# Optimization experiments

Measured on AMD Instinct MI355X. Metric: run time of the kernel, lower is better.

The kernel has to match this reference:

```python
import jax, jax.numpy as jnp
import numpy as np

HEADS = 8
DH = 160
LN_EPS = 1e-5


def _ln(x):
    m = jnp.mean(x, axis=-1, keepdims=True)
    v = jnp.var(x, axis=-1, keepdims=True)
    return (x - m) * jax.lax.rsqrt(v + LN_EPS)


def _adaln(x, table, w, b, t):
    # table[t]: [dim]; emb -> [2*dim]; chunk along dim 0 (scalar timestep)
    emb = jax.nn.silu(table[t]) @ w + b
    scale, shift = jnp.split(emb, 2)
    return _ln(x) * (1.0 + scale) + shift


def _attn(x, ctx, wq, wk, wv, wo, bo):
    B, S, _ = x.shape
    Sk = ctx.shape[1]
    q = (x @ wq).reshape(B, S, HEADS, DH).transpose(0, 2, 1, 3)    # [B,H,S,dh]
    k = (ctx @ wk).reshape(B, Sk, HEADS, DH).transpose(0, 2, 1, 3)
    v = (ctx @ wv).reshape(B, Sk, HEADS, DH).transpose(0, 2, 1, 3)
    scores = jnp.einsum('bhid,bhjd->bhij', q, k) * (DH ** -0.5)
    probs = jax.nn.softmax(scores, axis=-1)
    o = jnp.einsum('bhij,bhjd->bhid', probs, v)
    o = o.transpose(0, 2, 1, 3).reshape(B, S, HEADS * DH)
    return o @ wo + bo


def _ff(x, w1, b1, w2, b2):
    h, gate = jnp.split(x @ w1 + b1, 2, axis=-1)
    return (h * jax.nn.gelu(gate, approximate=False)) @ w2 + b2


def setup_inputs() -> dict:
    key = jax.random.key(0)
    ks = jax.random.split(key, 24)
    B, S, SC, DIM, CROSS, INNER = 2, 2048, 77, 1280, 768, 5120

    def w(k, shape, s=0.02):
        return jax.random.normal(k, shape, jnp.float32) * s

    return {
        'hidden_states': jax.random.normal(ks[0], (B, S, DIM), jnp.float32),
        'context': jax.random.normal(ks[1], (B, SC, CROSS), jnp.float32),
        'ada1_emb': w(ks[2], (1000, DIM)),
        'ada1_w': w(ks[3], (DIM, 2 * DIM)),
        'ada1_b': jnp.zeros((2 * DIM,), jnp.float32),
        'ada2_emb': w(ks[4], (1000, DIM)),
        'ada2_w': w(ks[5], (DIM, 2 * DIM)),
        'ada2_b': jnp.zeros((2 * DIM,), jnp.float32),
        'a1_wq': w(ks[6], (DIM, DIM)), 'a1_wk': w(ks[7], (DIM, DIM)),
        'a1_wv': w(ks[8], (DIM, DIM)), 'a1_wo': w(ks[9], (DIM, DIM)),
        'a1_bo': jnp.zeros((DIM,), jnp.float32),
        'a2_wq': w(ks[10], (DIM, DIM)), 'a2_wk': w(ks[11], (CROSS, DIM)),
        'a2_wv': w(ks[12], (CROSS, DIM)), 'a2_wo': w(ks[13], (DIM, DIM)),
        'a2_bo': jnp.zeros((DIM,), jnp.float32),
        'norm3_g': jnp.ones((DIM,), jnp.float32),
        'norm3_b': jnp.zeros((DIM,), jnp.float32),
        'ff_w1': w(ks[14], (DIM, 2 * INNER)),
        'ff_b1': jnp.zeros((2 * INNER,), jnp.float32),
        'ff_w2': w(ks[15], (INNER, DIM)),
        'ff_b2': jnp.zeros((DIM,), jnp.float32),
        'timestep': 500,
    }


def reference(hidden_states, context, ada1_emb, ada1_w, ada1_b, ada2_emb, ada2_w, ada2_b,
              a1_wq, a1_wk, a1_wv, a1_wo, a1_bo, a2_wq, a2_wk, a2_wv, a2_wo, a2_bo,
              norm3_g, norm3_b, ff_w1, ff_b1, ff_w2, ff_b2, timestep):
    x = hidden_states
    # self-attention with AdaLayerNorm
    h = _adaln(x, ada1_emb, ada1_w, ada1_b, timestep)
    x = x + _attn(h, h, a1_wq, a1_wk, a1_wv, a1_wo, a1_bo)
    # cross-attention with AdaLayerNorm
    h = _adaln(x, ada2_emb, ada2_w, ada2_b, timestep)
    x = x + _attn(h, context, a2_wq, a2_wk, a2_wv, a2_wo, a2_bo)
    # feed-forward with affine LayerNorm
    h = _ln(x) * norm3_g + norm3_b
    x = x + _ff(h, ff_w1, ff_b1, ff_w2, ff_b2)
    return x
```

## Files before the change

kernel.cpp:

```cpp
#include <hip/hip_runtime.h>

typedef __attribute__((ext_vector_type(8))) unsigned short ushort8;
typedef __attribute__((ext_vector_type(4))) float f32x4;
typedef __attribute__((ext_vector_type(8))) __bf16 bf16x8;
typedef unsigned short u16;

__device__ inline unsigned short f2bf(float f) {
  unsigned u = __float_as_uint(f);
  unsigned r = (u + 0x7fffu + ((u >> 16) & 1u)) >> 16;
  return (unsigned short)r;
}
__device__ inline float bf2f(unsigned short h) {
  return __uint_as_float(((unsigned)h) << 16);
}

__device__ __forceinline__ void gload_lds16(const void* g, void* l) {
  __builtin_amdgcn_global_load_lds(
      (const __attribute__((address_space(1))) void*)g,
      (__attribute__((address_space(3))) void*)l, 16, 0, 0);
}

__device__ __forceinline__ void decomp_bid(int nbx, int nby, int& z, int& bx, int& by) {
  int bid = blockIdx.x;
  const int nwg = gridDim.x;
  const int q8 = nwg >> 3, r8 = nwg & 7;
  const int xcd = bid & 7, i = bid >> 3;
  bid = (xcd < r8 ? xcd * (q8 + 1) : r8 * (q8 + 1) + (xcd - r8) * q8) + i;
  const int nbb = nbx * nby;
  z = bid / nbb;
  int rem = bid - z * nbb;
  if ((nby & 7) == 0) {
    const int chunk = nbx << 3;
    const int c = rem / chunk, w = rem - c * chunk;
    bx = w >> 3;
    by = (c << 3) + (w & 7);
  } else {
    by = rem / nbx;
    bx = rem - by * nbx;
  }
}

__global__ __launch_bounds__(512, 2) void flash_self(
    const u16* __restrict__ qkv, const u16* __restrict__ vtg, u16* __restrict__ o)
{
  __shared__ __align__(128) u16 Qs[128 * 168];
  __shared__ __align__(128) u16 Ks[2][64 * 168];
  __shared__ __align__(128) u16 Vs[2][160 * 64];
  __shared__ __align__(128) u16 Ps[128 * 64];

  const int tid = threadIdx.x;
  const int lane = tid & 63, wave = tid >> 6;
  const int r15 = lane & 15, kq = lane >> 4;
  const int z = blockIdx.x >> 4, qt = blockIdx.x & 15;
  const int b = z >> 3, hh = z & 7;
  const u16* Qg = qkv + ((long)(b * 2048 + qt * 128)) * 3840 + hh * 160;
  const u16* Kg = qkv + ((long)(b * 2048)) * 3840 + 1280 + hh * 160;
  const u16* Vg = vtg + (long)z * 160 * 2048;

  for (int c = tid; c < 2560; c += 512) {
    const int r = c / 20, e = (c % 20) * 8;
    *(ushort8*)&Qs[r * 168 + e] = *(const ushort8*)(Qg + (long)r * 3840 + e);
  }
  const int c0 = tid, c1 = tid + 512, c2 = tid + 1024;
  const bool has2 = (c2 < 1280);
  const int kR0 = c0 / 20, kE0 = (c0 % 20) * 8;
  const int kR1 = c1 / 20, kE1 = (c1 % 20) * 8;
  const int kR2 = has2 ? c2 / 20 : 0, kE2 = has2 ? (c2 % 20) * 8 : 0;
  const int vR0 = c0 >> 3, vG0 = c0 & 7;
  const int vR1 = c1 >> 3, vG1 = c1 & 7;
  const int vR2 = has2 ? (c2 >> 3) : 0, vG2 = has2 ? (c2 & 7) : 0;

  {
    ushort8 k0 = *(const ushort8*)(Kg + (long)kR0 * 3840 + kE0);
    ushort8 k1 = *(const ushort8*)(Kg + (long)kR1 * 3840 + kE1);
    ushort8 v0 = *(const ushort8*)(Vg + (long)vR0 * 2048 + vG0 * 8);
    ushort8 v1 = *(const ushort8*)(Vg + (long)vR1 * 2048 + vG1 * 8);
    *(ushort8*)&Ks[0][kR0 * 168 + kE0] = k0;
    *(ushort8*)&Ks[0][kR1 * 168 + kE1] = k1;
    *(ushort8*)&Vs[0][vR0 * 64 + ((vG0 ^ (vR0 & 7)) * 8)] = v0;
    *(ushort8*)&Vs[0][vR1 * 64 + ((vG1 ^ (vR1 & 7)) * 8)] = v1;
    if (has2) {
      ushort8 k2 = *(const ushort8*)(Kg + (long)kR2 * 3840 + kE2);
      ushort8 v2 = *(const ushort8*)(Vg + (long)vR2 * 2048 + vG2 * 8);
      *(ushort8*)&Ks[0][kR2 * 168 + kE2] = k2;
      *(ushort8*)&Vs[0][vR2 * 64 + ((vG2 ^ (vR2 & 7)) * 8)] = v2;
    }
  }
  __syncthreads();

  bf16x8 qf[5];
#pragma unroll
  for (int kf = 0; kf < 5; ++kf)
    qf[kf] = *(const bf16x8*)&Qs[(wave * 16 + r15) * 168 + kf * 32 + kq * 8];

  float m[4], l[4] = {0.f, 0.f, 0.f, 0.f};
#pragma unroll
  for (int t = 0; t < 4; ++t) m[t] = -1e30f;
  f32x4 accO[10] = {};
  const float SC = 0.07905694150420949f;

  ushort8 kr0, kr1, kr2, vr0, vr1, vr2;

  for (int step = 0; step < 32; ++step) {
    const int cur = step & 1;
    const bool nl = step < 31;
    if (nl) {
      const long kv1 = (long)(step + 1) * 64;
      kr0 = *(const ushort8*)(Kg + (kv1 + kR0) * 3840 + kE0);
      kr1 = *(const ushort8*)(Kg + (kv1 + kR1) * 3840 + kE1);
      vr0 = *(const ushort8*)(Vg + (long)vR0 * 2048 + kv1 + vG0 * 8);
      vr1 = *(const ushort8*)(Vg + (long)vR1 * 2048 + kv1 + vG1 * 8);
      if (has2) {
        kr2 = *(const ushort8*)(Kg + (kv1 + kR2) * 3840 + kE2);
        vr2 = *(const ushort8*)(Vg + (long)vR2 * 2048 + kv1 + vG2 * 8);
      }
    }
    f32x4 sa[4] = {};
#pragma unroll
    for (int nf = 0; nf < 4; ++nf)
#pragma unroll
      for (int kf = 0; kf < 5; ++kf) {
        const bf16x8 kfrag =
            *(const bf16x8*)&Ks[cur][(nf * 16 + r15) * 168 + kf * 32 + kq * 8];
        sa[nf] = __builtin_amdgcn_mfma_f32_16x16x32_bf16(qf[kf], kfrag, sa[nf], 0, 0, 0);
      }
    float corr[4];
#pragma unroll
    for (int t = 0; t < 4; ++t) {
      float tm = fmaxf(fmaxf(sa[0][t], sa[1][t]), fmaxf(sa[2][t], sa[3][t])) * SC;
      tm = fmaxf(tm, __shfl_xor(tm, 1, 64));
      tm = fmaxf(tm, __shfl_xor(tm, 2, 64));
      tm = fmaxf(tm, __shfl_xor(tm, 4, 64));
      tm = fmaxf(tm, __shfl_xor(tm, 8, 64));
      const float mn = fmaxf(m[t], tm);
      corr[t] = __expf(m[t] - mn);
      m[t] = mn;
    }
    const int qr0 = wave * 16 + kq * 4;
#pragma unroll
    for (int t = 0; t < 4; ++t) {
      float rs = 0.f;
      const int qr = qr0 + t;
#pragma unroll
      for (int nf = 0; nf < 4; ++nf) {
        const float p = __expf(sa[nf][t] * SC - m[t]);
        rs += p;
        const int col = r15 + nf * 16;
        Ps[qr * 64 + (((col >> 3) ^ (qr & 7)) * 8) + (col & 7)] = f2bf(p);
      }
      rs += __shfl_xor(rs, 1, 64);
      rs += __shfl_xor(rs, 2, 64);
      rs += __shfl_xor(rs, 4, 64);
      rs += __shfl_xor(rs, 8, 64);
      l[t] = l[t] * corr[t] + rs;
    }
#pragma unroll
    for (int j = 0; j < 10; ++j)
#pragma unroll
      for (int t = 0; t < 4; ++t) accO[j][t] *= corr[t];
    if (nl) {
      const int nxt = cur ^ 1;
      *(ushort8*)&Ks[nxt][kR0 * 168 + kE0] = kr0;
      *(ushort8*)&Ks[nxt][kR1 * 168 + kE1] = kr1;
      *(ushort8*)&Vs[nxt][vR0 * 64 + ((vG0 ^ (vR0 & 7)) * 8)] = vr0;
      *(ushort8*)&Vs[nxt][vR1 * 64 + ((vG1 ^ (vR1 & 7)) * 8)] = vr1;
      if (has2) {
        *(ushort8*)&Ks[nxt][kR2 * 168 + kE2] = kr2;
        *(ushort8*)&Vs[nxt][vR2 * 64 + ((vG2 ^ (vR2 & 7)) * 8)] = vr2;
      }
    }
    __syncthreads();
    const int arow = wave * 16 + r15;
    bf16x8 pf[2];
#pragma unroll
    for (int k2 = 0; k2 < 2; ++k2)
      pf[k2] = *(const bf16x8*)&Ps[arow * 64 + (((k2 * 4 + kq) ^ (arow & 7)) * 8)];
#pragma unroll
    for (int j = 0; j < 10; ++j)
#pragma unroll
      for (int k2 = 0; k2 < 2; ++k2) {
        const int vrow = j * 16 + r15;
        const bf16x8 vf =
            *(const bf16x8*)&Vs[cur][vrow * 64 + (((k2 * 4 + kq) ^ (vrow & 7)) * 8)];
        accO[j] = __builtin_amdgcn_mfma_f32_16x16x32_bf16(pf[k2], vf, accO[j], 0, 0, 0);
      }
    __syncthreads();
  }
  float inv[4];
#pragma unroll
  for (int t = 0; t < 4; ++t) inv[t] = 1.f / l[t];
  u16* orow = o + ((long)(b * 2048 + qt * 128)) * 1280 + hh * 160;
#pragma unroll
  for (int j = 0; j < 10; ++j)
#pragma unroll
    for (int t = 0; t < 4; ++t) {
      const int qr = wave * 16 + kq * 4 + t;
      orow[(long)qr * 1280 + j * 16 + r15] = f2bf(accO[j][t] * inv[t]);
    }
}

__global__ __launch_bounds__(512, 1) void flash_cross(
    const u16* __restrict__ q, const u16* __restrict__ kv, u16* __restrict__ o)
{
  __shared__ __align__(128) u16 Qs[128 * 168];
  __shared__ __align__(128) u16 Ks[80 * 168];
  __shared__ __align__(128) u16 Vts[160 * 104];
  __shared__ __align__(128) u16 Ps[128 * 104];

  const int tid = threadIdx.x;
  const int lane = tid & 63, wave = tid >> 6;
  const int r15 = lane & 15, kq = lane >> 4;
  const int z = blockIdx.x >> 4, qt = blockIdx.x & 15;
  const int b = z >> 3, hh = z & 7;
  const u16* Qg = q + ((long)(b * 2048 + qt * 128)) * 1280 + hh * 160;
  const u16* Kg = kv + (long)b * 77 * 2560 + hh * 160;
  const u16* Vg = Kg + 1280;

  for (int c = tid; c < 2560; c += 512) {
    const int r = c / 20, e = (c % 20) * 8;
    *(ushort8*)&Qs[r * 168 + e] = *(const ushort8*)(Qg + (long)r * 1280 + e);
  }
  for (int c = tid; c < 1540; c += 512) {
    const int r = c / 20, e = (c % 20) * 8;
    *(ushort8*)&Ks[r * 168 + e] = *(const ushort8*)(Kg + (long)r * 2560 + e);
  }
  for (int c = tid; c < 3 * 168; c += 512) Ks[77 * 168 + c] = 0;
  for (int c = tid; c < 77 * 160; c += 512) {
    const int s = c / 160, d = c - s * 160;
    Vts[d * 104 + s] = Vg[(long)s * 2560 + d];
  }
  for (int c = tid; c < 160 * 27; c += 512) {
    const int d = c / 27, cc = 77 + (c - d * 27);
    Vts[d * 104 + cc] = 0;
  }
  for (int c = tid; c < 128 * 16; c += 512) {
    const int r = c >> 4, cc = 80 + (c & 15);
    Ps[r * 104 + cc] = 0;
  }
  __syncthreads();

  const float SC = 0.07905694150420949f;
  bf16x8 qf[5];
#pragma unroll
  for (int kf = 0; kf < 5; ++kf)
    qf[kf] = *(const bf16x8*)&Qs[(wave * 16 + r15) * 168 + kf * 32 + kq * 8];
  f32x4 sa[5] = {};
#pragma unroll
  for (int nf = 0; nf < 5; ++nf)
#pragma unroll
    for (int kf = 0; kf < 5; ++kf) {
      const bf16x8 kfrag = *(const bf16x8*)&Ks[(nf * 16 + r15) * 168 + kf * 32 + kq * 8];
      sa[nf] = __builtin_amdgcn_mfma_f32_16x16x32_bf16(qf[kf], kfrag, sa[nf], 0, 0, 0);
    }
  float inv[4];
#pragma unroll
  for (int t = 0; t < 4; ++t) {
    float sv[5];
    float m = -1e30f;
#pragma unroll
    for (int nf = 0; nf < 5; ++nf) {
      const int col = nf * 16 + r15;
      sv[nf] = (col < 77) ? sa[nf][t] * SC : -1e30f;
      m = fmaxf(m, sv[nf]);
    }
    m = fmaxf(m, __shfl_xor(m, 1, 64));
    m = fmaxf(m, __shfl_xor(m, 2, 64));
    m = fmaxf(m, __shfl_xor(m, 4, 64));
    m = fmaxf(m, __shfl_xor(m, 8, 64));
    const int qr = wave * 16 + kq * 4 + t;
    float rs = 0.f;
#pragma unroll
    for (int nf = 0; nf < 5; ++nf) {
      const float p = __expf(sv[nf] - m);
      rs += p;
      Ps[qr * 104 + nf * 16 + r15] = f2bf(p);
    }
    rs += __shfl_xor(rs, 1, 64);
    rs += __shfl_xor(rs, 2, 64);
    rs += __shfl_xor(rs, 4, 64);
    rs += __shfl_xor(rs, 8, 64);
    inv[t] = 1.f / rs;
  }
  __syncthreads();
  const int arow = wave * 16 + r15;
  bf16x8 pf[3];
#pragma unroll
  for (int k2 = 0; k2 < 3; ++k2)
    pf[k2] = *(const bf16x8*)&Ps[arow * 104 + k2 * 32 + kq * 8];
  f32x4 accO[10] = {};
#pragma unroll
  for (int j = 0; j < 10; ++j)
#pragma unroll
    for (int k2 = 0; k2 < 3; ++k2) {
      const bf16x8 vf = *(const bf16x8*)&Vts[(j * 16 + r15) * 104 + k2 * 32 + kq * 8];
      accO[j] = __builtin_amdgcn_mfma_f32_16x16x32_bf16(pf[k2], vf, accO[j], 0, 0, 0);
    }
  u16* orow = o + ((long)(b * 2048 + qt * 128)) * 1280 + hh * 160;
#pragma unroll
  for (int j = 0; j < 10; ++j)
#pragma unroll
    for (int t = 0; t < 4; ++t) {
      const int qr = wave * 16 + kq * 4 + t;
      orow[(long)qr * 1280 + j * 16 + r15] = f2bf(accO[j][t] * inv[t]);
    }
}

__global__ __launch_bounds__(512, 4) void gemm64(
    const u16* __restrict__ A, long lda, long sAo, long sAi,
    const u16* __restrict__ B, long ldb, long sBo, long sBi,
    void* __restrict__ C, long ldc, long sCo, long sCi,
    const float* __restrict__ bias, const float* __restrict__ resid, long ldr,
    int M, int N, int K, int nbx, int Hdiv, float alpha, int outF32, int geglu)
{
  __shared__ __align__(128) char smem[65536];
  const int tid = threadIdx.x;
  const int lane = tid & 63, wave = tid >> 6;

  int z, bx, by;
  decomp_bid(nbx, M >> 7, z, bx, by);
  const int m0 = by << 7, n0 = bx << 7;
  const int zb = z / Hdiv, zh = z - zb * Hdiv;
  const u16* Ab = A + (long)zb * sAo + (long)zh * sAi;
  const u16* Bb = B + (long)zb * sBo + (long)zh * sBi;

  const int srow = tid >> 3;
  const int g8 = ((tid & 7) ^ (srow & 7)) * 8;
  long aoff[2], boff[2];
#pragma unroll
  for (int i = 0; i < 2; ++i) {
    aoff[i] = (long)(m0 + i * 64 + srow) * lda + g8;
    boff[i] = (long)(n0 + i * 64 + srow) * ldb + g8;
  }
  const int ldst = tid * 16;

  const int wm = (wave >> 2) * 64, wn = (wave & 3) * 32;
  const int r15 = lane & 15, kq = lane >> 4;
  const int offK0 = (kq ^ (lane & 7)) * 16;
  const int offK1 = ((4 + kq) ^ (lane & 7)) * 16;

  const int nt = K >> 6;

#define STAGE64(bufofs, k0)                                                       \
  do {                                                                            \
    _Pragma("unroll") for (int i = 0; i < 2; ++i)                                 \
        gload_lds16(Ab + aoff[i] + (k0), smem + (bufofs) + i * 8192 + ldst);      \
    _Pragma("unroll") for (int i = 0; i < 2; ++i)                                 \
        gload_lds16(Bb + boff[i] + (k0), smem + (bufofs) + 16384 + i * 8192 + ldst); \
  } while (0)

  STAGE64(0, 0);
  STAGE64(32768, 64);

  f32x4 acc[4][2] = {};

  for (int t = 0; t < nt; ++t) {
    const int cbuf = (t & 1) << 15;
    if (t < nt - 1) asm volatile("s_waitcnt vmcnt(4)" ::: "memory");
    else            asm volatile("s_waitcnt vmcnt(0)" ::: "memory");
    __builtin_amdgcn_s_barrier();

    bf16x8 bfr[2][2];
#pragma unroll
    for (int q = 0; q < 2; ++q) {
      if (q == 0) {
#pragma unroll
        for (int j = 0; j < 2; ++j) {
          const int bb = cbuf + 16384 + (wn + j * 16 + r15) * 128;
          bfr[j][0] = *(const bf16x8*)(smem + bb + offK0);
          bfr[j][1] = *(const bf16x8*)(smem + bb + offK1);
        }
      }
      bf16x8 af[2][2];
#pragma unroll
      for (int i2 = 0; i2 < 2; ++i2) {
        const int ab = cbuf + (wm + (q * 2 + i2) * 16 + r15) * 128;
        af[i2][0] = *(const bf16x8*)(smem + ab + offK0);
        af[i2][1] = *(const bf16x8*)(smem + ab + offK1);
      }
      __builtin_amdgcn_s_setprio(1);
#pragma unroll
      for (int kk = 0; kk < 2; ++kk)
#pragma unroll
        for (int i2 = 0; i2 < 2; ++i2)
#pragma unroll
          for (int j = 0; j < 2; ++j)
            acc[q * 2 + i2][j] = __builtin_amdgcn_mfma_f32_16x16x32_bf16(
                af[i2][kk], bfr[j][kk], acc[q * 2 + i2][j], 0, 0, 0);
      __builtin_amdgcn_s_setprio(0);
      __builtin_amdgcn_s_barrier();
    }
    if (t + 2 < nt) STAGE64(cbuf, (long)(t + 2) * 64);
  }
#undef STAGE64

  const long cbase = (long)zb * sCo + (long)zh * sCi;
  const int rb = (lane >> 4) * 4;
  if (geglu) {
    const int cH = n0 + wn + r15;
    const float bh = bias[cH], bg = bias[cH + 16];
    const int ocol = ((n0 + wn) >> 1) + r15;
#pragma unroll
    for (int i = 0; i < 4; ++i) {
#pragma unroll
      for (int tt = 0; tt < 4; ++tt) {
        const int grow = m0 + wm + i * 16 + rb + tt;
        const float hv = acc[i][0][tt] + bh;
        const float gv = acc[i][1][tt] + bg;
        const float gel = 0.5f * gv * (1.f + erff(gv * 0.7071067811865475f));
        ((u16*)C)[(long)grow * ldc + ocol] = f2bf(hv * gel);
      }
    }
    return;
  }
#pragma unroll
  for (int i = 0; i < 4; ++i) {
#pragma unroll
    for (int j = 0; j < 2; ++j) {
      const int gcol = n0 + wn + j * 16 + r15;
      if (gcol >= N) continue;
      const float bv = bias ? bias[gcol] : 0.f;
#pragma unroll
      for (int tt = 0; tt < 4; ++tt) {
        const int grow = m0 + wm + i * 16 + rb + tt;
        float val = acc[i][j][tt] * alpha + bv;
        if (resid) val += resid[(long)grow * ldr + gcol];
        const long cidx = cbase + (long)grow * ldc + gcol;
        if (outF32) ((float*)C)[cidx] = val;
        else ((u16*)C)[cidx] = f2bf(val);
      }
    }
  }
}

__global__ __launch_bounds__(256) void gemm_nt(
    const u16* __restrict__ A, long lda, long sAo, long sAi,
    const u16* __restrict__ B, long ldb, long sBo, long sBi,
    void* __restrict__ C, long ldc, long sCo, long sCi,
    const float* __restrict__ bias,
    const float* __restrict__ resid, long ldr,
    int M, int N, int K, int Hdiv, float alpha, int outF32)
{
  __shared__ u16 As[128 * 32];
  __shared__ u16 Bs[128 * 32];
  const int tid = threadIdx.x;
  const int z = blockIdx.z;
  const int zb = z / Hdiv, zh = z % Hdiv;
  const u16* Ab = A + (long)zb * sAo + (long)zh * sAi;
  const u16* Bb = B + (long)zb * sBo + (long)zh * sBi;
  const long cbase = (long)zb * sCo + (long)zh * sCi;
  const int m0 = blockIdx.y * 128, n0 = blockIdx.x * 128;
  const int lane = tid & 63, wave = tid >> 6;
  const int wm = (wave >> 1) * 64, wn = (wave & 1) * 64;
  const int r15 = lane & 15, kb = (lane >> 4) * 8;

  f32x4 acc[4][4] = {};

  for (int k0 = 0; k0 < K; k0 += 32) {
#pragma unroll
    for (int it = 0; it < 2; ++it) {
      const int c = tid + it * 256;
      const int row = c >> 2, ko = (c & 3) * 8;
      ushort8 va = {0, 0, 0, 0, 0, 0, 0, 0};
      const int gm = m0 + row;
      if (gm < M) va = *reinterpret_cast<const ushort8*>(Ab + (long)gm * lda + k0 + ko);
      *reinterpret_cast<ushort8*>(&As[row * 32 + ko]) = va;
      ushort8 vb = {0, 0, 0, 0, 0, 0, 0, 0};
      const int gn = n0 + row;
      if (gn < N) vb = *reinterpret_cast<const ushort8*>(Bb + (long)gn * ldb + k0 + ko);
      *reinterpret_cast<ushort8*>(&Bs[row * 32 + ko]) = vb;
    }
    __syncthreads();
    bf16x8 af[4], bfr[4];
#pragma unroll
    for (int i = 0; i < 4; ++i)
      af[i] = *reinterpret_cast<const bf16x8*>(&As[(wm + i * 16 + r15) * 32 + kb]);
#pragma unroll
    for (int j = 0; j < 4; ++j)
      bfr[j] = *reinterpret_cast<const bf16x8*>(&Bs[(wn + j * 16 + r15) * 32 + kb]);
#pragma unroll
    for (int i = 0; i < 4; ++i)
#pragma unroll
      for (int j = 0; j < 4; ++j)
        acc[i][j] = __builtin_amdgcn_mfma_f32_16x16x32_bf16(af[i], bfr[j], acc[i][j], 0, 0, 0);
    __syncthreads();
  }

  const int rb = (lane >> 4) * 4;
#pragma unroll
  for (int i = 0; i < 4; ++i) {
#pragma unroll
    for (int j = 0; j < 4; ++j) {
      const int gcol = n0 + wn + j * 16 + r15;
      if (gcol >= N) continue;
#pragma unroll
      for (int t = 0; t < 4; ++t) {
        const int grow = m0 + wm + i * 16 + rb + t;
        if (grow >= M) continue;
        float val = acc[i][j][t] * alpha;
        if (bias) val += bias[gcol];
        if (resid) val += resid[(long)grow * ldr + gcol];
        const long cidx = cbase + (long)grow * ldc + gcol;
        if (outF32) ((float*)C)[cidx] = val;
        else ((u16*)C)[cidx] = f2bf(val);
      }
    }
  }
}

__global__ void transpose_convert(const float* __restrict__ in,
                                  u16* __restrict__ out, int R, int C) {
  __shared__ float tile[32][33];
  const int c0 = blockIdx.x * 32, r0 = blockIdx.y * 32;
  const int tx = threadIdx.x, ty = threadIdx.y;
  for (int i = ty; i < 32; i += 8) {
    const int r = r0 + i, c = c0 + tx;
    tile[i][tx] = (r < R && c < C) ? in[(long)r * C + c] : 0.f;
  }
  __syncthreads();
  for (int i = ty; i < 32; i += 8) {
    const int c = c0 + i, r = r0 + tx;
    if (c < C && r < R) out[(long)c * R + r] = f2bf(tile[tx][i]);
  }
}

__global__ void tconv_ff1(const float* __restrict__ in, u16* __restrict__ out) {
  __shared__ float tile[32][33];
  const int r0 = blockIdx.y * 32;
  const int k0 = blockIdx.x * 32;
  const int w = r0 >> 5;
  const int tx = threadIdx.x, ty = threadIdx.y;
  const int src = (tx < 16) ? (w * 16 + tx) : (5120 + w * 16 + tx - 16);
  for (int i = ty; i < 32; i += 8)
    tile[i][tx] = in[(long)(k0 + i) * 10240 + src];
  __syncthreads();
  for (int i = ty; i < 32; i += 8)
    out[(long)(r0 + i) * 1280 + k0 + tx] = f2bf(tile[tx][i]);
}

__global__ void perm_b1(const float* __restrict__ b, float* __restrict__ bp) {
  const int r = blockIdx.x * 256 + threadIdx.x;
  if (r >= 10240) return;
  const int w = r >> 5, s = r & 31;
  bp[r] = b[(s < 16) ? (w * 16 + s) : (5120 + w * 16 + s - 16)];
}

__global__ void convert_bf16(const float* __restrict__ in,
                             u16* __restrict__ out, long n) {
  const long i = (long)blockIdx.x * 256 + threadIdx.x;
  if (i < n) out[i] = f2bf(in[i]);
}

__global__ __launch_bounds__(256) void adaln_emb(
    const float* __restrict__ t1, const float* __restrict__ w1, const float* __restrict__ b1,
    const float* __restrict__ t2, const float* __restrict__ w2, const float* __restrict__ b2,
    const int* __restrict__ tstep, float* __restrict__ e1, float* __restrict__ e2)
{
  const int which = blockIdx.y;
  const float* tb = which ? t2 : t1;
  const float* w = which ? w2 : w1;
  const float* bb = which ? b2 : b1;
  float* out = which ? e2 : e1;
  const int t = tstep[0];
  __shared__ float sil[1280];
  const int tid = threadIdx.x;
  for (int i = tid; i < 1280; i += 256) {
    const float xv = tb[(long)t * 1280 + i];
    sil[i] = xv / (1.f + expf(-xv));
  }
  __syncthreads();
  const int j = blockIdx.x * 256 + tid;
  float acc = bb[j];
  for (int k = 0; k < 1280; ++k) acc += sil[k] * w[(long)k * 2560 + j];
  out[j] = acc;
}

__global__ __launch_bounds__(256) void ln_mod(
    const float* __restrict__ x, u16* __restrict__ out,
    const float* __restrict__ emb, const float* __restrict__ g,
    const float* __restrict__ bv, int affine)
{
  const long row = blockIdx.x;
  const float* xr = x + row * 1280;
  const int tid = threadIdx.x;
  float v[5], s = 0.f, s2 = 0.f;
#pragma unroll
  for (int i = 0; i < 5; ++i) {
    const float t = xr[tid + i * 256];
    v[i] = t; s += t; s2 += t * t;
  }
  __shared__ float rs_[4], rs2_[4], bc[2];
  for (int off = 32; off; off >>= 1) {
    s += __shfl_down(s, off, 64);
    s2 += __shfl_down(s2, off, 64);
  }
  if ((tid & 63) == 0) { rs_[tid >> 6] = s; rs2_[tid >> 6] = s2; }
  __syncthreads();
  if (tid == 0) {
    const float S = rs_[0] + rs_[1] + rs_[2] + rs_[3];
    const float S2 = rs2_[0] + rs2_[1] + rs2_[2] + rs2_[3];
    const float mean = S * (1.f / 1280.f);
    const float var = S2 * (1.f / 1280.f) - mean * mean;
    bc[0] = mean; bc[1] = rsqrtf(var + 1e-5f);
  }
  __syncthreads();
  const float mean = bc[0], rstd = bc[1];
#pragma unroll
  for (int i = 0; i < 5; ++i) {
    const int c = tid + i * 256;
    const float ln = (v[i] - mean) * rstd;
    const float y = affine ? (ln * g[c] + bv[c]) : (ln * (1.f + emb[c]) + emb[1280 + c]);
    out[row * 1280 + c] = f2bf(y);
  }
}

__global__ void transpose_v_self(const u16* __restrict__ v, int ldv,
                                 u16* __restrict__ vt) {
  __shared__ u16 t[32][33];
  const int z = blockIdx.z, b = z >> 3, hh = z & 7;
  const int s0 = blockIdx.x * 32, d0 = blockIdx.y * 32;
  const int tx = threadIdx.x, ty = threadIdx.y;
  for (int i = ty; i < 32; i += 8) {
    const int d = d0 + tx;
    t[i][tx] = (d < 160) ? v[((long)(b * 2048 + s0 + i)) * ldv + hh * 160 + d]
                         : (u16)0;
  }
  __syncthreads();
  for (int i = ty; i < 32; i += 8) {
    const int d = d0 + i;
    if (d < 160) vt[((long)z * 160 + d) * 2048 + s0 + tx] = t[tx][i];
  }
}

extern "C" void kernel_launch(void* const* d_in, const int* in_sizes, int n_in,
                              void* d_out, int out_size, void* d_ws, size_t ws_size,
                              hipStream_t stream) {
  (void)in_sizes; (void)n_in; (void)out_size; (void)ws_size;

  const float* hidden   = (const float*)d_in[0];
  const float* context  = (const float*)d_in[1];
  const float* ada1_tab = (const float*)d_in[2];
  const float* ada1_w   = (const float*)d_in[3];
  const float* ada1_b   = (const float*)d_in[4];
  const float* ada2_tab = (const float*)d_in[5];
  const float* ada2_w   = (const float*)d_in[6];
  const float* ada2_b   = (const float*)d_in[7];
  const float* a1_wq = (const float*)d_in[8];
  const float* a1_wk = (const float*)d_in[9];
  const float* a1_wv = (const float*)d_in[10];
  const float* a1_wo = (const float*)d_in[11];
  const float* a1_bo = (const float*)d_in[12];
  const float* a2_wq = (const float*)d_in[13];
  const float* a2_wk = (const float*)d_in[14];
  const float* a2_wv = (const float*)d_in[15];
  const float* a2_wo = (const float*)d_in[16];
  const float* a2_bo = (const float*)d_in[17];
  const float* n3_g  = (const float*)d_in[18];
  const float* n3_b  = (const float*)d_in[19];
  const float* ff_w1 = (const float*)d_in[20];
  const float* ff_b1 = (const float*)d_in[21];
  const float* ff_w2 = (const float*)d_in[22];
  const float* ff_b2 = (const float*)d_in[23];
  const int*   tstep = (const int*)d_in[24];
  float* xout = (float*)d_out;

  char* base = (char*)d_ws;
  size_t off = 0;
  auto alloc = [&](size_t bytes) -> void* {
    void* p = base + off;
    off = (off + bytes + 255) & ~(size_t)255;
    return p;
  };
  u16* wqkvT = (u16*)alloc((size_t)3 * 1280 * 1280 * 2);
  u16* wo1T = (u16*)alloc((size_t)1280 * 1280 * 2);
  u16* wq2T = (u16*)alloc((size_t)1280 * 1280 * 2);
  u16* wkv2T = (u16*)alloc((size_t)2 * 1280 * 768 * 2);
  u16* wo2T = (u16*)alloc((size_t)1280 * 1280 * 2);
  u16* w1Tp = (u16*)alloc((size_t)10240 * 1280 * 2);
  u16* w2T  = (u16*)alloc((size_t)1280 * 5120 * 2);
  u16* ctxb = (u16*)alloc((size_t)154 * 768 * 2);
  float* emb1 = (float*)alloc(2560 * 4);
  float* emb2 = (float*)alloc(2560 * 4);
  float* b1p  = (float*)alloc(10240 * 4);
  u16* h   = (u16*)alloc((size_t)4096 * 1280 * 2);
  u16* qkv = (u16*)alloc((size_t)4096 * 3840 * 2);
  u16* vt  = (u16*)alloc((size_t)16 * 160 * 2048 * 2);
  u16* o   = (u16*)alloc((size_t)4096 * 1280 * 2);
  u16* kvx = (u16*)alloc((size_t)154 * 2560 * 2);
  u16* qc = qkv;
  u16* ffh = qkv;

  auto g64 = [&](const u16* A, long lda, long sAo, long sAi,
                 const u16* B, long ldb, long sBo, long sBi,
                 void* C, long ldc, long sCo, long sCi,
                 const float* bias, const float* resid, long ldr,
                 int M, int N, int K, int batch, int Hdiv, float alpha,
                 int outF32, int geglu) {
    const int nbx = (N + 127) >> 7;
    const int nwg = nbx * (M >> 7) * batch;
    gemm64<<<nwg, 512, 0, stream>>>(A, lda, sAo, sAi, B, ldb, sBo, sBi,
                                    C, ldc, sCo, sCi, bias, resid, ldr,
                                    M, N, K, nbx, Hdiv, alpha, outF32, geglu);
  };
  auto gemm = [&](const u16* A, long lda, long sAo, long sAi,
                  const u16* B, long ldb, long sBo, long sBi,
                  void* C, long ldc, long sCo, long sCi,
                  const float* bias, const float* resid, long ldr,
                  int M, int N, int K, int batch, int Hdiv, float alpha, int outF32) {
    dim3 g((N + 127) / 128, (M + 127) / 128, batch);
    gemm_nt<<<g, 256, 0, stream>>>(A, lda, sAo, sAi, B, ldb, sBo, sBi, C, ldc, sCo, sCi,
                                   bias, resid, ldr, M, N, K, Hdiv, alpha, outF32);
  };
  auto tconv = [&](const float* in, u16* out, int R, int C) {
    transpose_convert<<<dim3((C + 31) / 32, (R + 31) / 32), dim3(32, 8), 0, stream>>>(in, out, R, C);
  };

  tconv(a1_wq, wqkvT, 1280, 1280);
  tconv(a1_wk, wqkvT + (size_t)1280 * 1280, 1280, 1280);
  tconv(a1_wv, wqkvT + (size_t)2 * 1280 * 1280, 1280, 1280);
  tconv(a1_wo, wo1T, 1280, 1280);
  tconv(a2_wq, wq2T, 1280, 1280);
  tconv(a2_wk, wkv2T, 768, 1280);
  tconv(a2_wv, wkv2T + (size_t)1280 * 768, 768, 1280);
  tconv(a2_wo, wo2T, 1280, 1280);
  tconv_ff1<<<dim3(40, 320), dim3(32, 8), 0, stream>>>(ff_w1, w1Tp);
  perm_b1<<<40, 256, 0, stream>>>(ff_b1, b1p);
  tconv(ff_w2, w2T, 5120, 1280);
  {
    const long n = (long)154 * 768;
    convert_bf16<<<(int)((n + 255) / 256), 256, 0, stream>>>(context, ctxb, n);
  }
  adaln_emb<<<dim3(10, 2), 256, 0, stream>>>(ada1_tab, ada1_w, ada1_b,
                                             ada2_tab, ada2_w, ada2_b, tstep, emb1, emb2);

  u16* vs = qkv + 2560;

  ln_mod<<<4096, 256, 0, stream>>>(hidden, h, emb1, nullptr, nullptr, 0);
  g64(h, 1280, 0, 0, wqkvT, 1280, 0, 0, qkv, 3840, 0, 0,
      nullptr, nullptr, 0, 4096, 3840, 1280, 1, 1, 1.f, 0, 0);
  transpose_v_self<<<dim3(64, 5, 16), dim3(32, 8), 0, stream>>>(vs, 3840, vt);
  flash_self<<<256, 512, 0, stream>>>(qkv, vt, o);
  g64(o, 1280, 0, 0, wo1T, 1280, 0, 0, xout, 1280, 0, 0,
      a1_bo, hidden, 1280, 4096, 1280, 1280, 1, 1, 1.f, 1, 0);

  ln_mod<<<4096, 256, 0, stream>>>(xout, h, emb2, nullptr, nullptr, 0);
  g64(h, 1280, 0, 0, wq2T, 1280, 0, 0, qc, 1280, 0, 0,
      nullptr, nullptr, 0, 4096, 1280, 1280, 1, 1, 1.f, 0, 0);
  gemm(ctxb, 768, 0, 0, wkv2T, 768, 0, 0, kvx, 2560, 0, 0, nullptr, nullptr, 0,
       154, 2560, 768, 1, 1, 1.f, 0);
  flash_cross<<<256, 512, 0, stream>>>(qc, kvx, o);
  g64(o, 1280, 0, 0, wo2T, 1280, 0, 0, xout, 1280, 0, 0,
      a2_bo, xout, 1280, 4096, 1280, 1280, 1, 1, 1.f, 1, 0);

  ln_mod<<<4096, 256, 0, stream>>>(xout, h, nullptr, n3_g, n3_b, 1);
  g64(h, 1280, 0, 0, w1Tp, 1280, 0, 0, ffh, 5120, 0, 0,
      b1p, nullptr, 0, 4096, 10240, 1280, 1, 1, 1.f, 0, 1);
  g64(ffh, 5120, 0, 0, w2T, 5120, 0, 0, xout, 1280, 0, 0,
      ff_b2, xout, 1280, 4096, 1280, 5120, 1, 1, 1.f, 1, 0);
}
```

Measured before the change: 673.6 us.

## Add 256x256-tile GEMM kernel for the QKV and FF1 GEGLU projections

Adds a new GEMM kernel with 256x256 output tiles, 128KB of LDS double buffering and an 8-phase interleaved load/compute schedule. It replaces the 128x128 kernel for the wide QKV projection and the FF1 GEGLU projection, and the GEGLU epilogue moves into the new kernel. Larger tiles are meant to raise arithmetic intensity and cut global and LDS traffic per FLOP. The cost is one workgroup per CU, which lowers occupancy, and fewer workgroups overall: 240 for QKV and 640 for FF1, which may leave CUs idle on the tail wave.

```diff
diff --git a/kernel.cpp b/kernel.cpp
--- a/kernel.cpp
+++ b/kernel.cpp
@@ -305,12 +305,145 @@
     }
 }
 
+__global__ __launch_bounds__(512, 1) void gemm8p(
+    const u16* __restrict__ A, long lda, const u16* __restrict__ B, long ldb,
+    void* __restrict__ C, long ldc, const float* __restrict__ bias,
+    const float* __restrict__ resid, long ldr,
+    int M, int N, int K, int nbx, int outF32, int geglu)
+{
+  __shared__ __align__(128) char smem[131072];
+  const int tid = threadIdx.x;
+  const int lane = tid & 63, wave = tid >> 6;
+  const int wr = wave >> 2, wc = wave & 3;
+
+  int z, bx, by;
+  decomp_bid(nbx, M >> 8, z, bx, by);
+  const int m0 = by << 8, n0 = bx << 8;
+
+  const int srow = tid >> 3;
+  const int g8 = ((tid & 7) ^ (srow & 7)) * 8;
+  const int ldst = tid * 16;
+
+  const int r15 = lane & 15, kq = lane >> 4;
+  const int offK0 = (kq ^ (lane & 7)) * 16;
+  const int offK1 = ((4 + kq) ^ (lane & 7)) * 16;
+  const int abase = wr * 16384;
+  const int bbase = 32768 + (wc >> 1) * 16384;
+  const int brow0 = (wc & 1) * 64;
+
+  auto stA = [&](int cb, int h, long kt) {
+    const long k0 = kt * 64 + g8;
+    gload_lds16(A + (long)(m0 + h * 128 + srow) * lda + k0,
+                smem + cb + h * 16384 + ldst);
+    gload_lds16(A + (long)(m0 + h * 128 + 64 + srow) * lda + k0,
+                smem + cb + h * 16384 + 8192 + ldst);
+  };
+  auto stB = [&](int cb, int h, long kt) {
+    const long k0 = kt * 64 + g8;
+    gload_lds16(B + (long)(n0 + h * 128 + srow) * ldb + k0,
+                smem + cb + 32768 + h * 16384 + ldst);
+    gload_lds16(B + (long)(n0 + h * 128 + 64 + srow) * ldb + k0,
+                smem + cb + 32768 + h * 16384 + 8192 + ldst);
+  };
+
+  f32x4 acc[8][4] = {};
+
+  stA(0, 0, 0); stA(0, 1, 0); stB(0, 0, 0); stB(0, 1, 0);
+  stB(65536, 0, 1); stB(65536, 1, 1);
+  asm volatile("s_waitcnt vmcnt(4)" ::: "memory");
+
+#define PH(CB, P, STMT)                                                        \
+  {                                                                            \
+    __builtin_amdgcn_s_barrier();                                              \
+    STMT;                                                                      \
+    if ((P) == 0) {                                                            \
+      _Pragma("unroll") for (int j = 0; j < 4; ++j) {                          \
+        const int rbb = (CB) + bbase + (brow0 + j * 16 + r15) * 128;           \
+        bfr[j][0] = *(const bf16x8*)(smem + rbb + offK0);                      \
+        bfr[j][1] = *(const bf16x8*)(smem + rbb + offK1);                      \
+      }                                                                        \
+    }                                                                          \
+    bf16x8 af[2][2];                                                           \
+    _Pragma("unroll") for (int i2 = 0; i2 < 2; ++i2) {                         \
+      const int rab = (CB) + abase + ((P) * 32 + i2 * 16 + r15) * 128;         \
+      af[i2][0] = *(const bf16x8*)(smem + rab + offK0);                        \
+      af[i2][1] = *(const bf16x8*)(smem + rab + offK1);                        \
+    }                                                                          \
+    __builtin_amdgcn_s_setprio(1);                                             \
+    _Pragma("unroll") for (int kk = 0; kk < 2; ++kk)                           \
+      _Pragma("unroll") for (int i2 = 0; i2 < 2; ++i2)                         \
+        _Pragma("unroll") for (int j = 0; j < 4; ++j)                          \
+          acc[(P) * 2 + i2][j] = __builtin_amdgcn_mfma_f32_16x16x32_bf16(      \
+              af[i2][kk], bfr[j][kk], acc[(P) * 2 + i2][j], 0, 0, 0);          \
+    __builtin_amdgcn_s_setprio(0);                                             \
+  }
+
+  const int nI = K >> 7;
+  for (int t = 0; t < nI; ++t) {
+    const bool more = (t + 1 < nI);
+    const long k1 = 2 * t + 1, k2 = 2 * t + 2, k3 = 2 * t + 3;
+    bf16x8 bfr[4][2];
+    PH(0, 0, stA(65536, 0, k1))
+    PH(0, 1, stA(65536, 1, k1))
+    PH(0, 2, if (more) stB(0, 0, k2))
+    PH(0, 3, if (more) stB(0, 1, k2))
+    if (more) asm volatile("s_waitcnt vmcnt(4)" ::: "memory");
+    else      asm volatile("s_waitcnt vmcnt(0)" ::: "memory");
+    PH(65536, 0, if (more) stA(0, 0, k2))
+    PH(65536, 1, if (more) stA(0, 1, k2))
+    PH(65536, 2, if (more) stB(65536, 0, k3))
+    PH(65536, 3, if (more) stB(65536, 1, k3))
+    if (more) asm volatile("s_waitcnt vmcnt(4)" ::: "memory");
+  }
+#undef PH
+
+  const int rb = (lane >> 4) * 4;
+  if (geglu) {
+#pragma unroll
+    for (int jp = 0; jp < 2; ++jp) {
+      const float bh = bias[n0 + wc * 64 + jp * 32 + r15];
+      const float bg = bias[n0 + wc * 64 + jp * 32 + 16 + r15];
+      const int ocol = ((n0 + wc * 64) >> 1) + jp * 16 + r15;
+#pragma unroll
+      for (int i = 0; i < 8; ++i) {
+#pragma unroll
+        for (int tt = 0; tt < 4; ++tt) {
+          const int grow = m0 + wr * 128 + i * 16 + rb + tt;
+          const float hv = acc[i][jp * 2][tt] + bh;
+          const float gv = acc[i][jp * 2 + 1][tt] + bg;
+          const float gel = 0.5f * gv * (1.f + erff(gv * 0.7071067811865475f));
+          ((u16*)C)[(long)grow * ldc + ocol] = f2bf(hv * gel);
+        }
+      }
+    }
+    return;
+  }
+#pragma unroll
+  for (int i = 0; i < 8; ++i) {
+#pragma unroll
+    for (int j = 0; j < 4; ++j) {
+      const int gcol = n0 + wc * 64 + j * 16 + r15;
+      if (gcol >= N) continue;
+      const float bv = bias ? bias[gcol] : 0.f;
+#pragma unroll
+      for (int tt = 0; tt < 4; ++tt) {
+        const int grow = m0 + wr * 128 + i * 16 + rb + tt;
+        float val = acc[i][j][tt] + bv;
+        if (resid) val += resid[(long)grow * ldr + gcol];
+        const long cidx = (long)grow * ldc + gcol;
+        if (outF32) ((float*)C)[cidx] = val;
+        else ((u16*)C)[cidx] = f2bf(val);
+      }
+    }
+  }
+}
+
 __global__ __launch_bounds__(512, 4) void gemm64(
     const u16* __restrict__ A, long lda, long sAo, long sAi,
     const u16* __restrict__ B, long ldb, long sBo, long sBi,
     void* __restrict__ C, long ldc, long sCo, long sCi,
     const float* __restrict__ bias, const float* __restrict__ resid, long ldr,
-    int M, int N, int K, int nbx, int Hdiv, float alpha, int outF32, int geglu)
+    int M, int N, int K, int nbx, int Hdiv, float alpha, int outF32)
 {
   __shared__ __align__(128) char smem[65536];
   const int tid = threadIdx.x;
@@ -395,23 +528,6 @@
 
   const long cbase = (long)zb * sCo + (long)zh * sCi;
   const int rb = (lane >> 4) * 4;
-  if (geglu) {
-    const int cH = n0 + wn + r15;
-    const float bh = bias[cH], bg = bias[cH + 16];
-    const int ocol = ((n0 + wn) >> 1) + r15;
-#pragma unroll
-    for (int i = 0; i < 4; ++i) {
-#pragma unroll
-      for (int tt = 0; tt < 4; ++tt) {
-        const int grow = m0 + wm + i * 16 + rb + tt;
-        const float hv = acc[i][0][tt] + bh;
-        const float gv = acc[i][1][tt] + bg;
-        const float gel = 0.5f * gv * (1.f + erff(gv * 0.7071067811865475f));
-        ((u16*)C)[(long)grow * ldc + ocol] = f2bf(hv * gel);
-      }
-    }
-    return;
-  }
 #pragma unroll
   for (int i = 0; i < 4; ++i) {
 #pragma unroll
@@ -689,17 +805,24 @@
   u16* qc = qkv;
   u16* ffh = qkv;
 
+  auto g8p = [&](const u16* A, long lda, const u16* B, long ldb,
+                 void* C, long ldc, const float* bias, const float* resid, long ldr,
+                 int M, int N, int K, int outF32, int geglu) {
+    const int nbx = N >> 8;
+    const int nwg = nbx * (M >> 8);
+    gemm8p<<<nwg, 512, 0, stream>>>(A, lda, B, ldb, C, ldc, bias, resid, ldr,
+                                    M, N, K, nbx, outF32, geglu);
+  };
   auto g64 = [&](const u16* A, long lda, long sAo, long sAi,
                  const u16* B, long ldb, long sBo, long sBi,
                  void* C, long ldc, long sCo, long sCi,
                  const float* bias, const float* resid, long ldr,
-                 int M, int N, int K, int batch, int Hdiv, float alpha,
-                 int outF32, int geglu) {
+                 int M, int N, int K, int batch, int Hdiv, float alpha, int outF32) {
     const int nbx = (N + 127) >> 7;
     const int nwg = nbx * (M >> 7) * batch;
     gemm64<<<nwg, 512, 0, stream>>>(A, lda, sAo, sAi, B, ldb, sBo, sBi,
                                     C, ldc, sCo, sCi, bias, resid, ldr,
-                                    M, N, K, nbx, Hdiv, alpha, outF32, geglu);
+                                    M, N, K, nbx, Hdiv, alpha, outF32);
   };
   auto gemm = [&](const u16* A, long lda, long sAo, long sAi,
                   const u16* B, long ldb, long sBo, long sBi,
@@ -735,25 +858,25 @@
   u16* vs = qkv + 2560;
 
   ln_mod<<<4096, 256, 0, stream>>>(hidden, h, emb1, nullptr, nullptr, 0);
-  g64(h, 1280, 0, 0, wqkvT, 1280, 0, 0, qkv, 3840, 0, 0,
-      nullptr, nullptr, 0, 4096, 3840, 1280, 1, 1, 1.f, 0, 0);
+  g8p(h, 1280, wqkvT, 1280, qkv, 3840, nullptr, nullptr, 0,
+      4096, 3840, 1280, 0, 0);
   transpose_v_self<<<dim3(64, 5, 16), dim3(32, 8), 0, stream>>>(vs, 3840, vt);
   flash_self<<<256, 512, 0, stream>>>(qkv, vt, o);
   g64(o, 1280, 0, 0, wo1T, 1280, 0, 0, xout, 1280, 0, 0,
-      a1_bo, hidden, 1280, 4096, 1280, 1280, 1, 1, 1.f, 1, 0);
+      a1_bo, hidden, 1280, 4096, 1280, 1280, 1, 1, 1.f, 1);
 
   ln_mod<<<4096, 256, 0, stream>>>(xout, h, emb2, nullptr, nullptr, 0);
   g64(h, 1280, 0, 0, wq2T, 1280, 0, 0, qc, 1280, 0, 0,
-      nullptr, nullptr, 0, 4096, 1280, 1280, 1, 1, 1.f, 0, 0);
+      nullptr, nullptr, 0, 4096, 1280, 1280, 1, 1, 1.f, 0);
   gemm(ctxb, 768, 0, 0, wkv2T, 768, 0, 0, kvx, 2560, 0, 0, nullptr, nullptr, 0,
        154, 2560, 768, 1, 1, 1.f, 0);
   flash_cross<<<256, 512, 0, stream>>>(qc, kvx, o);
   g64(o, 1280, 0, 0, wo2T, 1280, 0, 0, xout, 1280, 0, 0,
-      a2_bo, xout, 1280, 4096, 1280, 1280, 1, 1, 1.f, 1, 0);
+      a2_bo, xout, 1280, 4096, 1280, 1280, 1, 1, 1.f, 1);
 
   ln_mod<<<4096, 256, 0, stream>>>(xout, h, nullptr, n3_g, n3_b, 1);
-  g64(h, 1280, 0, 0, w1Tp, 1280, 0, 0, ffh, 5120, 0, 0,
-      b1p, nullptr, 0, 4096, 10240, 1280, 1, 1, 1.f, 0, 1);
+  g8p(h, 1280, w1Tp, 1280, ffh, 5120, b1p, nullptr, 0,
+      4096, 10240, 1280, 0, 1);
   g64(ffh, 5120, 0, 0, w2T, 5120, 0, 0, xout, 1280, 0, 0,
-      ff_b2, xout, 1280, 4096, 1280, 5120, 1, 1, 1.f, 1, 0);
-}
+      ff_b2, xout, 1280, 4096, 1280, 5120, 1, 1, 1.f, 1);
+}
```

After: 683.6 us. Within noise of the previous version (+1.5%).
